# Optimization experiments

Hardware: AMD Instinct MI355X
Metric: run time of the kernel (lower is better)

Reference implementation:

```python
import jax, jax.numpy as jnp
import numpy as np

N_SHOTS, N_SAMPLES, IMG = 10, 192, 256
M = N_SHOTS * N_SAMPLES  # 1920 k-space samples


def _radial_traj():
    # mri-nufft initialize_2D_radial: uniform spoke angles over pi,
    # radii in [-0.5, 0.5) with N_SAMPLES points per spoke.
    r = (np.arange(N_SAMPLES) - N_SAMPLES / 2) / N_SAMPLES
    ang = np.pi * np.arange(N_SHOTS) / N_SHOTS
    kx = np.cos(ang)[:, None] * r[None, :]
    ky = np.sin(ang)[:, None] * r[None, :]
    return np.stack([kx, ky], axis=-1).reshape(-1, 2).astype(np.float32)


def _phase_mats(samples):
    # Separable NDFT phase factors: exp(-2i*pi*k_x*i), exp(-2i*pi*k_y*j)
    grid = jnp.arange(IMG, dtype=jnp.float32) - IMG / 2  # centered pixel coords
    Ax = jnp.exp(-2j * jnp.pi * samples[:, 0:1] * grid[None, :]).astype(jnp.complex64)  # (M, IMG)
    Ay = jnp.exp(-2j * jnp.pi * samples[:, 1:2] * grid[None, :]).astype(jnp.complex64)  # (M, IMG)
    return Ax, Ay


def _pipe_density(samples, n_iter=10):
    # Pipe & Menon density compensation: w <- w / |F F^H w| (density=True in gpunufft).
    Ax, Ay = _phase_mats(samples)
    w = jnp.ones(M, jnp.complex64)
    for _ in range(n_iter):
        t = Ax.conj() * w[:, None]                    # (M, IMG)
        img = jnp.einsum('mi,mj->ij', t, Ay.conj())   # F^H w, (IMG, IMG)
        back = jnp.einsum('mi,ij,mj->m', Ax, img, Ay) # F F^H w, (M,)
        w = w / jnp.maximum(jnp.abs(back), 1e-12).astype(jnp.complex64)
    return jnp.abs(w).astype(jnp.float32)


def setup_inputs() -> dict:
    key = jax.random.key(0)
    k1, k2 = jax.random.split(key)
    B, C = 64, 1
    x_real = jax.random.normal(k1, (B, C, IMG, IMG), dtype=jnp.float32)
    x_imag = jax.random.normal(k2, (B, C, IMG, IMG), dtype=jnp.float32)
    samples = jnp.asarray(_radial_traj())
    density = _pipe_density(samples)
    return {"x_real": x_real, "x_imag": x_imag, "samples": samples, "density": density}


def reference(x_real, x_imag, samples, density):
    x = (x_real + 1j * x_imag).astype(jnp.complex64)  # (B, C, IMG, IMG)
    Ax, Ay = _phase_mats(samples)
    # Forward NUFFT (type-2 NDFT): kspace[b,c,m] = sum_ij Ax[m,i] Ay[m,j] x[b,c,i,j]
    t = jnp.einsum('mi,bcij->bcmj', Ax, x)            # (B, C, M, IMG)
    kspace = jnp.einsum('mj,bcmj->bcm', Ay, t)        # (B, C, M)
    # Density-compensated adjoint NUFFT (type-1 NDFT)
    kw = kspace * density.astype(jnp.complex64)
    u = jnp.einsum('mi,bcm->bcmi', Ax.conj(), kw)     # (B, C, M, IMG)
    adj = jnp.einsum('mj,bcmi->bcij', Ay.conj(), u) / (IMG * IMG)
    return jnp.stack([adj.real, adj.imag], axis=-1)   # (B, C, IMG, IMG, 2)
```

## Files before the change

### kernel.cpp

```cpp
#include <hip/hip_runtime.h>
#include <hip/hip_bf16.h>
#include <hip/hip_fp16.h>

constexpr int IMG_ = 256;
constexpr int M_   = 1920;
constexpr int B_   = 64;
constexpr int MI_  = M_ * IMG_;
constexpr int IMG2 = IMG_ * IMG_;

typedef _Float16 half8 __attribute__((ext_vector_type(8)));
typedef float    floatx4 __attribute__((ext_vector_type(4)));

__device__ __forceinline__ void gll16(const _Float16* g, _Float16* l) {
  __builtin_amdgcn_global_load_lds(
      (const __attribute__((address_space(1))) void*)g,
      (__attribute__((address_space(3))) void*)l, 16, 0, 0);
}

constexpr int PH1_N = MI_ / 256;
constexpr int PH2_N = 8 * IMG_;
constexpr int XT_N  = 8 * 8 * B_;

__global__ __launch_bounds__(256) void prep_k(
    const float* __restrict__ samples,
    const float* __restrict__ xr, const float* __restrict__ xi,
    _Float16* __restrict__ axh_r, _Float16* __restrict__ axh_i,
    _Float16* __restrict__ ayh_r, _Float16* __restrict__ ayh_i,
    _Float16* __restrict__ axtc_r, _Float16* __restrict__ axtc_i,
    _Float16* __restrict__ aytc_r, _Float16* __restrict__ aytc_i,
    _Float16* __restrict__ xth_r, _Float16* __restrict__ xth_i) {
  __shared__ float tr[32][33], ti[32][33];
  const int t = threadIdx.x;
  const int n = blockIdx.x;

  if (n < PH1_N) {
    int idx = n * 256 + t;
    int m = idx >> 8;
    int i = idx & 255;
    float g  = (float)i - 128.0f;
    float kx = samples[2 * m + 0];
    float ky = samples[2 * m + 1];
    float sx, cx, sy, cy;
    sincospif(-2.0f * kx * g, &sx, &cx);
    sincospif(-2.0f * ky * g, &sy, &cy);
    axh_r[idx] = (_Float16)cx; axh_i[idx] = (_Float16)sx;
    ayh_r[idx] = (_Float16)cy; ayh_i[idx] = (_Float16)sy;
  } else if (n < PH1_N + PH2_N) {
    int nn = n - PH1_N;
    int m = (nn & 7) * 256 + t;
    int i = nn >> 3;
    if (m < M_) {
      float g  = (float)i - 128.0f;
      float kx = samples[2 * m + 0];
      float ky = samples[2 * m + 1];
      float sx, cx, sy, cy;
      sincospif(-2.0f * kx * g, &sx, &cx);
      sincospif(-2.0f * ky * g, &sy, &cy);
      int o = i * M_ + m;
      axtc_r[o] = (_Float16)cx; axtc_i[o] = (_Float16)(-sx);
      aytc_r[o] = (_Float16)cy; aytc_i[o] = (_Float16)(-sy);
    }
  } else {
    int nn = n - PH1_N - PH2_N;
    const int b  = nn >> 6;
    const int i0 = (nn & 7) * 32, j0 = ((nn >> 3) & 7) * 32;
    const int r = t >> 5, c = t & 31;
#pragma unroll
    for (int k = 0; k < 4; ++k) {
      int row = r + k * 8;
      tr[row][c] = xr[(size_t)b * IMG2 + (i0 + row) * IMG_ + j0 + c];
      ti[row][c] = xi[(size_t)b * IMG2 + (i0 + row) * IMG_ + j0 + c];
    }
    __syncthreads();
#pragma unroll
    for (int k = 0; k < 4; ++k) {
      int row = r + k * 8;
      xth_r[(size_t)b * IMG2 + (j0 + row) * IMG_ + i0 + c] = (_Float16)tr[c][row];
      xth_i[(size_t)b * IMG2 + (j0 + row) * IMG_ + i0 + c] = (_Float16)ti[c][row];
    }
  }
}


__global__ __launch_bounds__(256, 3) void fwd_k(
    const _Float16* __restrict__ axh_r, const _Float16* __restrict__ axh_i,
    const _Float16* __restrict__ ayh_r, const _Float16* __restrict__ ayh_i,
    const _Float16* __restrict__ xth_r, const _Float16* __restrict__ xth_i,
    const float* __restrict__ density,
    _Float16* __restrict__ kwh_r, _Float16* __restrict__ kwh_i) {
  __shared__ _Float16 lds[2][12288];
  __shared__ float2 scr[4][64];

  const int t  = threadIdx.x;
  const int w  = t >> 6;
  const int l  = t & 63;
  const int lr = l & 15;
  const int q  = l >> 4;

  const int n   = blockIdx.x;
  const int xcd = n & 7;
  const int r   = n >> 3;
  const int b   = xcd + 8 * (r / 30);
  const int m0  = (r % 30) * 64;

  const int srow   = l >> 2;
  const int schunk = (l & 3) ^ ((l >> 3) & 3);
  const int gA     = srow * IMG_ + schunk * 8;
  const int rc     = (q ^ ((lr >> 1) & 3)) << 3;

  const floatx4 z4 = {0.f, 0.f, 0.f, 0.f};
  floatx4 accr[4][2], acci[4][2];
#pragma unroll
  for (int mt = 0; mt < 4; ++mt)
#pragma unroll
    for (int jt = 0; jt < 2; ++jt) { accr[mt][jt] = z4; acci[mt][jt] = z4; }

  auto stage = [&](int buf, int s) {
    const int jc  = s >> 3;
    const int col = (s & 7) * 32;
    _Float16* L = lds[buf];
    const size_t offA = (size_t)(m0 + w * 16) * IMG_ + col + gA;
    gll16(axh_r + offA, L + 0    + w * 512);
    gll16(axh_i + offA, L + 2048 + w * 512);
    const size_t offB = (size_t)b * IMG2 + (size_t)(jc * 128 + w * 32) * IMG_ + col + gA;
    gll16(xth_r + offB,             L + 4096 + w * 1024);
    gll16(xth_r + offB + 16 * IMG_, L + 4096 + w * 1024 + 512);
    gll16(xth_i + offB,             L + 8192 + w * 1024);
    gll16(xth_i + offB + 16 * IMG_, L + 8192 + w * 1024 + 512);
  };

  auto compute = [&](int buf) {
    const _Float16* L = lds[buf];
    half8 br[2], bi[2], nbi[2];
#pragma unroll
    for (int jt = 0; jt < 2; ++jt) {
      const int ro = (w * 32 + jt * 16 + lr) * 32 + rc;
      br[jt]  = *(const half8*)&L[4096 + ro];
      bi[jt]  = *(const half8*)&L[8192 + ro];
      nbi[jt] = -bi[jt];
    }
#pragma unroll
    for (int mt = 0; mt < 4; ++mt) {
      const int ro = (mt * 16 + lr) * 32 + rc;
      half8 ar = *(const half8*)&L[0 + ro];
      half8 ai = *(const half8*)&L[2048 + ro];
#pragma unroll
      for (int jt = 0; jt < 2; ++jt) {
        accr[mt][jt] = __builtin_amdgcn_mfma_f32_16x16x32_f16(ar, br[jt],  accr[mt][jt], 0, 0, 0);
        accr[mt][jt] = __builtin_amdgcn_mfma_f32_16x16x32_f16(ai, nbi[jt], accr[mt][jt], 0, 0, 0);
        acci[mt][jt] = __builtin_amdgcn_mfma_f32_16x16x32_f16(ar, bi[jt],  acci[mt][jt], 0, 0, 0);
        acci[mt][jt] = __builtin_amdgcn_mfma_f32_16x16x32_f16(ai, br[jt],  acci[mt][jt], 0, 0, 0);
      }
    }
  };

  auto epi = [&](int jc) {
#pragma unroll
    for (int mt = 0; mt < 4; ++mt) {
      float kr[4] = {}, ki[4] = {};
#pragma unroll
      for (int jt = 0; jt < 2; ++jt) {
        const int j = jc * 128 + w * 32 + jt * 16 + lr;
#pragma unroll
        for (int reg = 0; reg < 4; ++reg) {
          const int m = m0 + mt * 16 + q * 4 + reg;
          const float yr = (float)ayh_r[m * IMG_ + j];
          const float yi = (float)ayh_i[m * IMG_ + j];
          const float tr = accr[mt][jt][reg], ti = acci[mt][jt][reg];
          kr[reg] = fmaf(yr, tr, fmaf(-yi, ti, kr[reg]));
          ki[reg] = fmaf(yr, ti, fmaf(yi, tr, ki[reg]));
        }
        accr[mt][jt] = z4;
        acci[mt][jt] = z4;
      }
#pragma unroll
      for (int reg = 0; reg < 4; ++reg)
#pragma unroll
        for (int off = 1; off < 16; off <<= 1) {
          kr[reg] += __shfl_xor(kr[reg], off);
          ki[reg] += __shfl_xor(ki[reg], off);
        }
      if (lr == 0) {
#pragma unroll
        for (int reg = 0; reg < 4; ++reg) {
          const int ml = mt * 16 + q * 4 + reg;
          if (jc == 0) {
            scr[w][ml] = make_float2(kr[reg], ki[reg]);
          } else {
            float2 p = scr[w][ml];
            scr[w][ml] = make_float2(p.x + kr[reg], p.y + ki[reg]);
          }
        }
      }
    }
  };

  stage(0, 0);
  __syncthreads();
#pragma unroll
  for (int s = 0; s < 16; ++s) {
    const int buf = s & 1;
    if (s < 15) stage(buf ^ 1, s + 1);
    compute(buf);
    if (s == 7) epi(0);
    __syncthreads();
  }
  epi(1);
  __syncthreads();

  if (t < 64) {
    float sr = 0.f, si = 0.f;
#pragma unroll
    for (int ww = 0; ww < 4; ++ww) {
      const float2 p = scr[ww][t];
      sr += p.x; si += p.y;
    }
    const int m = m0 + t;
    const float d = density[m];
    kwh_r[b * M_ + m] = (_Float16)(sr * d);
    kwh_i[b * M_ + m] = (_Float16)(si * d);
  }
}

__global__ __launch_bounds__(256, 3) void adj_k(
    const _Float16* __restrict__ axtc_r, const _Float16* __restrict__ axtc_i,
    const _Float16* __restrict__ aytc_r, const _Float16* __restrict__ aytc_i,
    const _Float16* __restrict__ kwh_r, const _Float16* __restrict__ kwh_i,
    float* __restrict__ out) {
  __shared__ _Float16 lds[2][8192];

  const int t  = threadIdx.x;
  const int w  = t >> 6;
  const int l  = t & 63;
  const int lr = l & 15;
  const int q  = l >> 4;
  const int wi = w >> 1;
  const int wj = w & 1;

  const int n     = blockIdx.x;
  const int xcd   = n & 7;
  const int r     = n >> 3;
  const int combo = xcd + 8 * (r >> 6);
  const int b     = r & 63;
  const int i0    = (combo >> 2) * 64;
  const int j0    = (combo & 3) * 64;

  const int srow   = l >> 2;
  const int schunk = (l & 3) ^ ((l >> 3) & 3);
  const int gA     = srow * M_ + schunk * 8;
  const int rc     = (q ^ ((lr >> 1) & 3)) << 3;

  const int wrow = t >> 2;
  const int wseg = t & 3;
  const int wsc  = wseg ^ ((wrow >> 1) & 3);

  const floatx4 z4 = {0.f, 0.f, 0.f, 0.f};
  floatx4 accr[2][2], acci[2][2];
#pragma unroll
  for (int mt = 0; mt < 2; ++mt)
#pragma unroll
    for (int jt = 0; jt < 2; ++jt) { accr[mt][jt] = z4; acci[mt][jt] = z4; }

  uint4 Yr, Yi, Cr, Ci;

  auto stageA = [&](int buf, int s) {
    const int mc = s * 32;
    _Float16* L = lds[buf];
    const size_t off = (size_t)(i0 + w * 16) * M_ + mc + gA;
    gll16(axtc_r + off, L + 0    + w * 512);
    gll16(axtc_i + off, L + 2048 + w * 512);
  };

  auto loadW = [&](int s) {
    const int mc = s * 32 + wsc * 8;
    const size_t oy = (size_t)(j0 + wrow) * M_ + mc;
    const size_t oc = (size_t)b * M_ + mc;
    Yr = *(const uint4*)&aytc_r[oy];
    Yi = *(const uint4*)&aytc_i[oy];
    Cr = *(const uint4*)&kwh_r[oc];
    Ci = *(const uint4*)&kwh_i[oc];
  };

  auto writeW = [&](int buf) {
    __half2 Wr[4], Wi2[4];
    const __half2* yr = (const __half2*)&Yr; const __half2* yi = (const __half2*)&Yi;
    const __half2* cr = (const __half2*)&Cr; const __half2* ci = (const __half2*)&Ci;
#pragma unroll
    for (int e = 0; e < 4; ++e) {
      Wr[e]  = __hsub2(__hmul2(cr[e], yr[e]), __hmul2(ci[e], yi[e]));
      Wi2[e] = __hfma2(cr[e], yi[e], __hmul2(ci[e], yr[e]));
    }
    _Float16* Lr = lds[buf] + 4096;
    _Float16* Li = lds[buf] + 6144;
    const int o = wrow * 32 + wseg * 8;
    *(uint4*)&Lr[o] = *(const uint4*)&Wr[0];
    *(uint4*)&Li[o] = *(const uint4*)&Wi2[0];
  };

  auto compute = [&](int buf) {
    const _Float16* L = lds[buf];
    half8 br[2], bi[2], nbi[2];
#pragma unroll
    for (int jt = 0; jt < 2; ++jt) {
      const int ro = (wj * 32 + jt * 16 + lr) * 32 + rc;
      br[jt]  = *(const half8*)&L[4096 + ro];
      bi[jt]  = *(const half8*)&L[6144 + ro];
      nbi[jt] = -bi[jt];
    }
#pragma unroll
    for (int mt = 0; mt < 2; ++mt) {
      const int ro = (wi * 32 + mt * 16 + lr) * 32 + rc;
      half8 ar = *(const half8*)&L[0 + ro];
      half8 ai = *(const half8*)&L[2048 + ro];
#pragma unroll
      for (int jt = 0; jt < 2; ++jt) {
        accr[mt][jt] = __builtin_amdgcn_mfma_f32_16x16x32_f16(ar, br[jt],  accr[mt][jt], 0, 0, 0);
        accr[mt][jt] = __builtin_amdgcn_mfma_f32_16x16x32_f16(ai, nbi[jt], accr[mt][jt], 0, 0, 0);
        acci[mt][jt] = __builtin_amdgcn_mfma_f32_16x16x32_f16(ar, bi[jt],  acci[mt][jt], 0, 0, 0);
        acci[mt][jt] = __builtin_amdgcn_mfma_f32_16x16x32_f16(ai, br[jt],  acci[mt][jt], 0, 0, 0);
      }
    }
  };

  loadW(0);
  stageA(0, 0);
  writeW(0);
  __syncthreads();
#pragma unroll 2
  for (int s = 0; s < 60; ++s) {
    const int buf = s & 1;
    if (s < 59) { stageA(buf ^ 1, s + 1); loadW(s + 1); }
    compute(buf);
    if (s < 59) writeW(buf ^ 1);
    __syncthreads();
  }

  const float sc = 1.0f / (float)IMG2;
#pragma unroll
  for (int mt = 0; mt < 2; ++mt)
#pragma unroll
    for (int jt = 0; jt < 2; ++jt) {
      const int jg = j0 + wj * 32 + jt * 16 + lr;
#pragma unroll
      for (int reg = 0; reg < 4; ++reg) {
        const int ig = i0 + wi * 32 + mt * 16 + q * 4 + reg;
        float2 v = make_float2(accr[mt][jt][reg] * sc, acci[mt][jt][reg] * sc);
        *(float2*)&out[((size_t)(b * IMG_ + ig) * IMG_ + jg) * 2] = v;
      }
    }
}

extern "C" void kernel_launch(void* const* d_in, const int* in_sizes, int n_in,
                              void* d_out, int out_size, void* d_ws, size_t ws_size,
                              hipStream_t stream) {
  (void)in_sizes; (void)n_in; (void)out_size; (void)ws_size;

  const float* xr      = (const float*)d_in[0];
  const float* xi      = (const float*)d_in[1];
  const float* samples = (const float*)d_in[2];
  const float* density = (const float*)d_in[3];
  float* out = (float*)d_out;

  _Float16* f = (_Float16*)d_ws;
  _Float16* axh_r  = f + 0 * MI_;
  _Float16* axh_i  = f + 1 * MI_;
  _Float16* ayh_r  = f + 2 * MI_;
  _Float16* ayh_i  = f + 3 * MI_;
  _Float16* axtc_r = f + 4 * MI_;
  _Float16* axtc_i = f + 5 * MI_;
  _Float16* aytc_r = f + 6 * MI_;
  _Float16* aytc_i = f + 7 * MI_;
  _Float16* kwh_r  = f + 8 * MI_;
  _Float16* kwh_i  = kwh_r + B_ * M_;

  _Float16* xth_r = (_Float16*)d_out;
  _Float16* xth_i = xth_r + (size_t)B_ * IMG2;

  prep_k<<<PH1_N + PH2_N + XT_N, 256, 0, stream>>>(
      samples, xr, xi, axh_r, axh_i, ayh_r, ayh_i,
      axtc_r, axtc_i, aytc_r, aytc_i, xth_r, xth_i);
  fwd_k<<<1920, 256, 0, stream>>>(axh_r, axh_i, ayh_r, ayh_i,
                                  xth_r, xth_i, density, kwh_r, kwh_i);
  adj_k<<<1024, 256, 0, stream>>>(axtc_r, axtc_i, aytc_r, aytc_i,
                                  kwh_r, kwh_i, out);
}
```

Before: 276.7 us.

## Split forward NDFT over j-halves and build adjoint B operand in registers

The forward kernel is split across the two j-column halves, doubling the block count. Each block writes fp32 partial k-space sums to scratch, and a new small kernel combines them and applies density. The adjoint kernel no longer stages the density-weighted Ay operand through LDS; each lane loads Ay and kspace directly and forms the MFMA B fragments in registers, which halves LDS use. This costs an extra launch and a scratch round trip, and the adjoint does redundant global loads across waves.

```diff
diff --git a/kernel.cpp b/kernel.cpp
--- a/kernel.cpp
+++ b/kernel.cpp
@@ -86,10 +86,8 @@
     const _Float16* __restrict__ axh_r, const _Float16* __restrict__ axh_i,
     const _Float16* __restrict__ ayh_r, const _Float16* __restrict__ ayh_i,
     const _Float16* __restrict__ xth_r, const _Float16* __restrict__ xth_i,
-    const float* __restrict__ density,
-    _Float16* __restrict__ kwh_r, _Float16* __restrict__ kwh_i) {
+    float2* __restrict__ kpart) {
   __shared__ _Float16 lds[2][12288];
-  __shared__ float2 scr[4][64];
 
   const int t  = threadIdx.x;
   const int w  = t >> 6;
@@ -97,11 +95,13 @@
   const int lr = l & 15;
   const int q  = l >> 4;
 
-  const int n   = blockIdx.x;
-  const int xcd = n & 7;
-  const int r   = n >> 3;
-  const int b   = xcd + 8 * (r / 30);
-  const int m0  = (r % 30) * 64;
+  const int n     = blockIdx.x;
+  const int r     = n >> 3;
+  const int b     = (n & 7) + 8 * (r / 60);
+  const int inner = r % 60;
+  const int m0    = (inner % 30) * 64;
+  const int jc    = inner / 30;
+  const int j0    = jc * 128;
 
   const int srow   = l >> 2;
   const int schunk = (l & 3) ^ ((l >> 3) & 3);
@@ -116,13 +116,12 @@
     for (int jt = 0; jt < 2; ++jt) { accr[mt][jt] = z4; acci[mt][jt] = z4; }
 
   auto stage = [&](int buf, int s) {
-    const int jc  = s >> 3;
-    const int col = (s & 7) * 32;
+    const int col = s * 32;
     _Float16* L = lds[buf];
     const size_t offA = (size_t)(m0 + w * 16) * IMG_ + col + gA;
     gll16(axh_r + offA, L + 0    + w * 512);
     gll16(axh_i + offA, L + 2048 + w * 512);
-    const size_t offB = (size_t)b * IMG2 + (size_t)(jc * 128 + w * 32) * IMG_ + col + gA;
+    const size_t offB = (size_t)b * IMG2 + (size_t)(j0 + w * 32) * IMG_ + col + gA;
     gll16(xth_r + offB,             L + 4096 + w * 1024);
     gll16(xth_r + offB + 16 * IMG_, L + 4096 + w * 1024 + 512);
     gll16(xth_i + offB,             L + 8192 + w * 1024);
@@ -154,72 +153,74 @@
     }
   };
 
-  auto epi = [&](int jc) {
-#pragma unroll
-    for (int mt = 0; mt < 4; ++mt) {
-      float kr[4] = {}, ki[4] = {};
-#pragma unroll
-      for (int jt = 0; jt < 2; ++jt) {
-        const int j = jc * 128 + w * 32 + jt * 16 + lr;
-#pragma unroll
-        for (int reg = 0; reg < 4; ++reg) {
-          const int m = m0 + mt * 16 + q * 4 + reg;
-          const float yr = (float)ayh_r[m * IMG_ + j];
-          const float yi = (float)ayh_i[m * IMG_ + j];
-          const float tr = accr[mt][jt][reg], ti = acci[mt][jt][reg];
-          kr[reg] = fmaf(yr, tr, fmaf(-yi, ti, kr[reg]));
-          ki[reg] = fmaf(yr, ti, fmaf(yi, tr, ki[reg]));
-        }
-        accr[mt][jt] = z4;
-        acci[mt][jt] = z4;
-      }
-#pragma unroll
-      for (int reg = 0; reg < 4; ++reg)
-#pragma unroll
-        for (int off = 1; off < 16; off <<= 1) {
-          kr[reg] += __shfl_xor(kr[reg], off);
-          ki[reg] += __shfl_xor(ki[reg], off);
-        }
-      if (lr == 0) {
-#pragma unroll
-        for (int reg = 0; reg < 4; ++reg) {
-          const int ml = mt * 16 + q * 4 + reg;
-          if (jc == 0) {
-            scr[w][ml] = make_float2(kr[reg], ki[reg]);
-          } else {
-            float2 p = scr[w][ml];
-            scr[w][ml] = make_float2(p.x + kr[reg], p.y + ki[reg]);
-          }
-        }
-      }
-    }
-  };
-
   stage(0, 0);
   __syncthreads();
 #pragma unroll
-  for (int s = 0; s < 16; ++s) {
+  for (int s = 0; s < 8; ++s) {
     const int buf = s & 1;
-    if (s < 15) stage(buf ^ 1, s + 1);
+    if (s < 7) stage(buf ^ 1, s + 1);
     compute(buf);
-    if (s == 7) epi(0);
     __syncthreads();
   }
-  epi(1);
+
+  float kr[4][4] = {}, ki[4][4] = {};
+#pragma unroll
+  for (int mt = 0; mt < 4; ++mt)
+#pragma unroll
+    for (int jt = 0; jt < 2; ++jt) {
+      const int j = j0 + w * 32 + jt * 16 + lr;
+#pragma unroll
+      for (int reg = 0; reg < 4; ++reg) {
+        const int m = m0 + mt * 16 + q * 4 + reg;
+        const float yr = (float)ayh_r[m * IMG_ + j];
+        const float yi = (float)ayh_i[m * IMG_ + j];
+        const float tr = accr[mt][jt][reg], ti = acci[mt][jt][reg];
+        kr[mt][reg] = fmaf(yr, tr, fmaf(-yi, ti, kr[mt][reg]));
+        ki[mt][reg] = fmaf(yr, ti, fmaf(yi, tr, ki[mt][reg]));
+      }
+    }
+
+#pragma unroll
+  for (int mt = 0; mt < 4; ++mt)
+#pragma unroll
+    for (int reg = 0; reg < 4; ++reg)
+#pragma unroll
+      for (int off = 1; off < 16; off <<= 1) {
+        kr[mt][reg] += __shfl_xor(kr[mt][reg], off);
+        ki[mt][reg] += __shfl_xor(ki[mt][reg], off);
+      }
+
+  float2* scr = (float2*)&lds[0][0];
+  if (lr == 0) {
+#pragma unroll
+    for (int mt = 0; mt < 4; ++mt)
+#pragma unroll
+      for (int reg = 0; reg < 4; ++reg)
+        scr[w * 64 + mt * 16 + q * 4 + reg] = make_float2(kr[mt][reg], ki[mt][reg]);
+  }
   __syncthreads();
-
   if (t < 64) {
     float sr = 0.f, si = 0.f;
 #pragma unroll
     for (int ww = 0; ww < 4; ++ww) {
-      const float2 p = scr[ww][t];
+      const float2 p = scr[ww * 64 + t];
       sr += p.x; si += p.y;
     }
-    const int m = m0 + t;
-    const float d = density[m];
-    kwh_r[b * M_ + m] = (_Float16)(sr * d);
-    kwh_i[b * M_ + m] = (_Float16)(si * d);
-  }
+    kpart[((size_t)jc * B_ + b) * M_ + m0 + t] = make_float2(sr, si);
+  }
+}
+
+__global__ __launch_bounds__(256) void comb_k(
+    const float2* __restrict__ kpart, const float* __restrict__ density,
+    _Float16* __restrict__ kwh_r, _Float16* __restrict__ kwh_i) {
+  const int idx = blockIdx.x * 256 + threadIdx.x;
+  if (idx >= B_ * M_) return;
+  const int m = idx % M_;
+  const float2 p0 = kpart[idx];
+  const float2 p1 = kpart[(size_t)B_ * M_ + idx];
+  const float d = density[m];
+  kwh_r[idx] = (_Float16)((p0.x + p1.x) * d);
+  kwh_i[idx] = (_Float16)((p0.y + p1.y) * d);
 }
 
 __global__ __launch_bounds__(256, 3) void adj_k(
@@ -227,7 +228,7 @@
     const _Float16* __restrict__ aytc_r, const _Float16* __restrict__ aytc_i,
     const _Float16* __restrict__ kwh_r, const _Float16* __restrict__ kwh_i,
     float* __restrict__ out) {
-  __shared__ _Float16 lds[2][8192];
+  __shared__ _Float16 lds[2][4096];
 
   const int t  = threadIdx.x;
   const int w  = t >> 6;
@@ -250,9 +251,9 @@
   const int gA     = srow * M_ + schunk * 8;
   const int rc     = (q ^ ((lr >> 1) & 3)) << 3;
 
-  const int wrow = t >> 2;
-  const int wseg = t & 3;
-  const int wsc  = wseg ^ ((wrow >> 1) & 3);
+  const size_t yrow0 = (size_t)(j0 + wj * 32 + 0 * 16 + lr) * M_;
+  const size_t yrow1 = (size_t)(j0 + wj * 32 + 1 * 16 + lr) * M_;
+  const size_t cbase = (size_t)b * M_;
 
   const floatx4 z4 = {0.f, 0.f, 0.f, 0.f};
   floatx4 accr[2][2], acci[2][2];
@@ -261,7 +262,7 @@
 #pragma unroll
     for (int jt = 0; jt < 2; ++jt) { accr[mt][jt] = z4; acci[mt][jt] = z4; }
 
-  uint4 Yr, Yi, Cr, Ci;
+  uint4 Yr[2], Yi[2], Cr, Ci;
 
   auto stageA = [&](int buf, int s) {
     const int mc = s * 32;
@@ -271,42 +272,35 @@
     gll16(axtc_i + off, L + 2048 + w * 512);
   };
 
-  auto loadW = [&](int s) {
-    const int mc = s * 32 + wsc * 8;
-    const size_t oy = (size_t)(j0 + wrow) * M_ + mc;
-    const size_t oc = (size_t)b * M_ + mc;
-    Yr = *(const uint4*)&aytc_r[oy];
-    Yi = *(const uint4*)&aytc_i[oy];
-    Cr = *(const uint4*)&kwh_r[oc];
-    Ci = *(const uint4*)&kwh_i[oc];
-  };
-
-  auto writeW = [&](int buf) {
-    __half2 Wr[4], Wi2[4];
-    const __half2* yr = (const __half2*)&Yr; const __half2* yi = (const __half2*)&Yi;
-    const __half2* cr = (const __half2*)&Cr; const __half2* ci = (const __half2*)&Ci;
-#pragma unroll
-    for (int e = 0; e < 4; ++e) {
-      Wr[e]  = __hsub2(__hmul2(cr[e], yr[e]), __hmul2(ci[e], yi[e]));
-      Wi2[e] = __hfma2(cr[e], yi[e], __hmul2(ci[e], yr[e]));
-    }
-    _Float16* Lr = lds[buf] + 4096;
-    _Float16* Li = lds[buf] + 6144;
-    const int o = wrow * 32 + wseg * 8;
-    *(uint4*)&Lr[o] = *(const uint4*)&Wr[0];
-    *(uint4*)&Li[o] = *(const uint4*)&Wi2[0];
+  auto loadY = [&](int s) {
+    const int mc = s * 32 + q * 8;
+    Yr[0] = *(const uint4*)&aytc_r[yrow0 + mc];
+    Yi[0] = *(const uint4*)&aytc_i[yrow0 + mc];
+    Yr[1] = *(const uint4*)&aytc_r[yrow1 + mc];
+    Yi[1] = *(const uint4*)&aytc_i[yrow1 + mc];
+    Cr    = *(const uint4*)&kwh_r[cbase + mc];
+    Ci    = *(const uint4*)&kwh_i[cbase + mc];
   };
 
   auto compute = [&](int buf) {
+    half8 br[2], bi2[2], nbi[2];
+#pragma unroll
+    for (int jt = 0; jt < 2; ++jt) {
+      __half2 Wr[4], Wi4[4];
+      const __half2* yr = (const __half2*)&Yr[jt];
+      const __half2* yi = (const __half2*)&Yi[jt];
+      const __half2* cr = (const __half2*)&Cr;
+      const __half2* ci = (const __half2*)&Ci;
+#pragma unroll
+      for (int e = 0; e < 4; ++e) {
+        Wr[e]  = __hsub2(__hmul2(cr[e], yr[e]), __hmul2(ci[e], yi[e]));
+        Wi4[e] = __hfma2(cr[e], yi[e], __hmul2(ci[e], yr[e]));
+      }
+      br[jt]  = *(const half8*)&Wr[0];
+      bi2[jt] = *(const half8*)&Wi4[0];
+      nbi[jt] = -bi2[jt];
+    }
     const _Float16* L = lds[buf];
-    half8 br[2], bi[2], nbi[2];
-#pragma unroll
-    for (int jt = 0; jt < 2; ++jt) {
-      const int ro = (wj * 32 + jt * 16 + lr) * 32 + rc;
-      br[jt]  = *(const half8*)&L[4096 + ro];
-      bi[jt]  = *(const half8*)&L[6144 + ro];
-      nbi[jt] = -bi[jt];
-    }
 #pragma unroll
     for (int mt = 0; mt < 2; ++mt) {
       const int ro = (wi * 32 + mt * 16 + lr) * 32 + rc;
@@ -316,22 +310,21 @@
       for (int jt = 0; jt < 2; ++jt) {
         accr[mt][jt] = __builtin_amdgcn_mfma_f32_16x16x32_f16(ar, br[jt],  accr[mt][jt], 0, 0, 0);
         accr[mt][jt] = __builtin_amdgcn_mfma_f32_16x16x32_f16(ai, nbi[jt], accr[mt][jt], 0, 0, 0);
-        acci[mt][jt] = __builtin_amdgcn_mfma_f32_16x16x32_f16(ar, bi[jt],  acci[mt][jt], 0, 0, 0);
+        acci[mt][jt] = __builtin_amdgcn_mfma_f32_16x16x32_f16(ar, bi2[jt], acci[mt][jt], 0, 0, 0);
         acci[mt][jt] = __builtin_amdgcn_mfma_f32_16x16x32_f16(ai, br[jt],  acci[mt][jt], 0, 0, 0);
       }
     }
   };
 
-  loadW(0);
+  loadY(0);
   stageA(0, 0);
-  writeW(0);
   __syncthreads();
 #pragma unroll 2
   for (int s = 0; s < 60; ++s) {
     const int buf = s & 1;
-    if (s < 59) { stageA(buf ^ 1, s + 1); loadW(s + 1); }
+    if (s < 59) stageA(buf ^ 1, s + 1);
     compute(buf);
-    if (s < 59) writeW(buf ^ 1);
+    if (s < 59) loadY(s + 1);
     __syncthreads();
   }
 
@@ -375,12 +368,14 @@
 
   _Float16* xth_r = (_Float16*)d_out;
   _Float16* xth_i = xth_r + (size_t)B_ * IMG2;
+  float2*   kpart = (float2*)(xth_i + (size_t)B_ * IMG2);
 
   prep_k<<<PH1_N + PH2_N + XT_N, 256, 0, stream>>>(
       samples, xr, xi, axh_r, axh_i, ayh_r, ayh_i,
       axtc_r, axtc_i, aytc_r, aytc_i, xth_r, xth_i);
-  fwd_k<<<1920, 256, 0, stream>>>(axh_r, axh_i, ayh_r, ayh_i,
-                                  xth_r, xth_i, density, kwh_r, kwh_i);
+  fwd_k<<<3840, 256, 0, stream>>>(axh_r, axh_i, ayh_r, ayh_i,
+                                  xth_r, xth_i, kpart);
+  comb_k<<<(B_ * M_ + 255) / 256, 256, 0, stream>>>(kpart, density, kwh_r, kwh_i);
   adj_k<<<1024, 256, 0, stream>>>(axtc_r, axtc_i, aytc_r, aytc_i,
                                   kwh_r, kwh_i, out);
 }
```

After: 322.1 us. 1.16x slower.
